# Performance work log

Hardware: AMD Instinct MI355X
Metric: run time of the kernel (lower is better)

The kernel has to match this reference:

```python
import jax, jax.numpy as jnp
import numpy as np

S = 14
STEP = 1.0 / S
LAMBDA_COORD = 7.0
LAMBDA_NOOBJ = 0.2
LAMBDA_CLS = 1.5
EPS = 1e-06


def _abs_coords(boxes):
    # boxes: [N, S, S, 2, 5] -> [N, S, S, 2, 4] (x1,y1,x2,y2)
    ys, xs = jnp.meshgrid(jnp.arange(S, dtype=boxes.dtype), jnp.arange(S, dtype=boxes.dtype), indexing='ij')
    xg = xs[None, :, :, None]
    yg = ys[None, :, :, None]
    cx = (boxes[..., 0] + xg) * STEP
    cy = (boxes[..., 1] + yg) * STEP
    w = boxes[..., 2]
    h = boxes[..., 3]
    return jnp.stack([cx - w / 2, cy - h / 2, cx + w / 2, cy + h / 2], axis=-1)


def _iou(b1, b2):
    x1 = jnp.maximum(b1[..., 0], b2[..., 0])
    y1 = jnp.maximum(b1[..., 1], b2[..., 1])
    x2 = jnp.minimum(b1[..., 2], b2[..., 2])
    y2 = jnp.minimum(b1[..., 3], b2[..., 3])
    inter = jnp.clip(x2 - x1, 0) * jnp.clip(y2 - y1, 0)
    a1 = (b1[..., 2] - b1[..., 0]) * (b1[..., 3] - b1[..., 1])
    a2 = (b2[..., 2] - b2[..., 0]) * (b2[..., 3] - b2[..., 1])
    return inter / (a1 + a2 - inter + EPS)


def _ciou_loss(b1, b2):
    iou = _iou(b1, b2)
    cx1 = (b1[..., 0] + b1[..., 2]) / 2
    cy1 = (b1[..., 1] + b1[..., 3]) / 2
    cx2 = (b2[..., 0] + b2[..., 2]) / 2
    cy2 = (b2[..., 1] + b2[..., 3]) / 2
    center_dist = (cx1 - cx2) ** 2 + (cy1 - cy2) ** 2
    xc1 = jnp.minimum(b1[..., 0], b2[..., 0])
    yc1 = jnp.minimum(b1[..., 1], b2[..., 1])
    xc2 = jnp.maximum(b1[..., 2], b2[..., 2])
    yc2 = jnp.maximum(b1[..., 3], b2[..., 3])
    outer_diag = (xc2 - xc1) ** 2 + (yc2 - yc1) ** 2 + EPS
    w1 = jnp.clip(b1[..., 2] - b1[..., 0], EPS)
    h1 = jnp.clip(b1[..., 3] - b1[..., 1], EPS)
    w2 = jnp.clip(b2[..., 2] - b2[..., 0], EPS)
    h2 = jnp.clip(b2[..., 3] - b2[..., 1], EPS)
    v = (4.0 / jnp.pi ** 2) * (jnp.arctan(w2 / h2) - jnp.arctan(w1 / h1)) ** 2
    alpha = v / (1 - iou + v + EPS)
    ciou = iou - center_dist / outer_diag - alpha * v
    scale = jnp.clip(2 - w2 * h2, 1.0)
    return (1 - ciou) * scale


def setup_inputs() -> dict:
    key = jax.random.key(0)
    k1, k2 = jax.random.split(key)
    N = 4096
    pred = jax.random.uniform(k1, (N, S, S, 30), dtype=jnp.float32)
    target = jax.random.uniform(k2, (N, S, S, 30), dtype=jnp.float32)
    return {"pred": pred, "target": target}


def reference(pred, target):
    N = pred.shape[0]
    tb = target[..., :10].reshape(N, S, S, 2, 5)
    pb = pred[..., :10].reshape(N, S, S, 2, 5)
    tcls = target[..., 10:]
    pcls = pred[..., 10:]

    obj = tb[..., 4] > 0                      # [N,S,S,2]
    pabs = _abs_coords(pb)                    # [N,S,S,2,4]
    tabs = _abs_coords(tb)

    # responsible-box assignment: IoU of both pred boxes vs target box 0
    ious = _iou(pabs, tabs[..., 0:1, :])      # [N,S,S,2]
    max_i = jnp.argmax(ious, axis=-1)         # first-max tie-break, same as torch
    resp = max_i[..., None] == jnp.arange(2)  # [N,S,S,2] bool
    obj = obj & resp
    noobj = ~obj

    pconf = pb[..., 4]
    tconf = tb[..., 4]
    se = (pconf - tconf) ** 2
    noobj_loss = jnp.sum(se * noobj)
    obj_loss = jnp.sum(se * obj)

    bbox_loss = jnp.sum(_ciou_loss(pabs, tabs) * obj)

    sig = jnp.any(obj, axis=-1)               # [N,S,S]
    # torch F.binary_cross_entropy clamps log terms at -100
    logp = jnp.clip(jnp.log(pcls), -100.0)
    log1mp = jnp.clip(jnp.log1p(-pcls), -100.0)
    bce = -(tcls * logp + (1 - tcls) * log1mp)
    class_loss = jnp.sum(bce * sig[..., None]) * LAMBDA_CLS

    loss = obj_loss + LAMBDA_NOOBJ * noobj_loss + LAMBDA_COORD * bbox_loss + class_loss
    return loss / N
```

## Files before the change

### kernel.cpp

```cpp
#include <hip/hip_runtime.h>
#include <math.h>

namespace {
constexpr int SG = 14;
constexpr int NCELLS = 4096 * SG * SG;
constexpr int CPB = 64;
constexpr int NBLK = NCELLS / CPB;
constexpr int NBINS = 1024;
constexpr int BYTES_PER_BLK = CPB * 30 * 4;
constexpr float STEPF = 1.0f / 14.0f;
constexpr float EPSF = 1e-6f;
constexpr float L_COORD = 7.0f;
constexpr float L_NOOBJ = 0.2f;
constexpr float L_CLS = 1.5f;
constexpr float INV_N = 1.0f / 4096.0f;
constexpr float FOUR_OVER_PI2 = 4.0f / (float)(M_PI * M_PI);
}

#define AS1 __attribute__((address_space(1)))
#define AS3 __attribute__((address_space(3)))

__device__ __forceinline__ void gl_lds16(const void* g, void* l) {
  __builtin_amdgcn_global_load_lds((const AS1 unsigned int*)g, (AS3 unsigned int*)l, 16, 0, 0);
}
__device__ __forceinline__ void gl_lds4(const void* g, void* l) {
  __builtin_amdgcn_global_load_lds((const AS1 unsigned int*)g, (AS3 unsigned int*)l, 4, 0, 0);
}

struct Box { float x1, y1, x2, y2; };

__device__ __forceinline__ float iou_fn(const Box& a, const Box& b) {
  float ix1 = fmaxf(a.x1, b.x1);
  float iy1 = fmaxf(a.y1, b.y1);
  float ix2 = fminf(a.x2, b.x2);
  float iy2 = fminf(a.y2, b.y2);
  float inter = fmaxf(ix2 - ix1, 0.0f) * fmaxf(iy2 - iy1, 0.0f);
  float a1 = (a.x2 - a.x1) * (a.y2 - a.y1);
  float a2 = (b.x2 - b.x1) * (b.y2 - b.y1);
  return __fdividef(inter, a1 + a2 - inter + EPSF);
}

__device__ __forceinline__ float bce_term(float pc, float tc) {
  const float lg   = fmaxf(__logf(pc), -100.0f);
  const float l1mp = fmaxf(__logf(1.0f - pc), -100.0f);
  return -(tc * lg + (1.0f - tc) * l1mp);
}

__global__ __launch_bounds__(64) void yolo_k1(const float* __restrict__ pred,
                                              const float* __restrict__ tgt,
                                              float* __restrict__ bins) {
  __shared__ __align__(16) float pb[CPB * 30];
  __shared__ __align__(16) float tb[CPB * 30];

  const int lane = threadIdx.x;
  const size_t base = (size_t)blockIdx.x * BYTES_PER_BLK;
  const char* gp = (const char*)pred + base;
  const char* gt = (const char*)tgt + base;
  char* lp = (char*)pb;
  char* lt = (char*)tb;

#pragma unroll
  for (int j = 0; j < 7; ++j) {
    gl_lds16(gp + j * 1024 + lane * 16, lp + j * 1024);
    gl_lds16(gt + j * 1024 + lane * 16, lt + j * 1024);
  }
#pragma unroll
  for (int j = 0; j < 2; ++j) {
    gl_lds4(gp + 7168 + j * 256 + lane * 4, lp + 7168 + j * 256);
    gl_lds4(gt + 7168 + j * 256 + lane * 4, lt + 7168 + j * 256);
  }
  asm volatile("s_waitcnt vmcnt(0)" ::: "memory");

  const float2* pl = reinterpret_cast<const float2*>(pb + lane * 30);
  const float2* tl = reinterpret_cast<const float2*>(tb + lane * 30);

  float p[10], t[10];
#pragma unroll
  for (int k = 0; k < 5; ++k) {
    const float2 v = pl[k]; p[2 * k] = v.x; p[2 * k + 1] = v.y;
    const float2 u = tl[k]; t[2 * k] = u.x; t[2 * k + 1] = u.y;
  }

  const int cell = blockIdx.x * CPB + lane;
  const int rem = cell % (SG * SG);
  const float gx = (float)(rem % SG);
  const float gy = (float)(rem / SG);

  Box pa0, pa1, ta0, ta1;
  {
    float cx = (p[0] + gx) * STEPF, cy = (p[1] + gy) * STEPF, w = p[2], h = p[3];
    pa0 = {cx - 0.5f * w, cy - 0.5f * h, cx + 0.5f * w, cy + 0.5f * h};
    cx = (p[5] + gx) * STEPF; cy = (p[6] + gy) * STEPF; w = p[7]; h = p[8];
    pa1 = {cx - 0.5f * w, cy - 0.5f * h, cx + 0.5f * w, cy + 0.5f * h};
    cx = (t[0] + gx) * STEPF; cy = (t[1] + gy) * STEPF; w = t[2]; h = t[3];
    ta0 = {cx - 0.5f * w, cy - 0.5f * h, cx + 0.5f * w, cy + 0.5f * h};
    cx = (t[5] + gx) * STEPF; cy = (t[6] + gy) * STEPF; w = t[7]; h = t[8];
    ta1 = {cx - 0.5f * w, cy - 0.5f * h, cx + 0.5f * w, cy + 0.5f * h};
  }

  const float iou0 = iou_fn(pa0, ta0);
  const float iou1 = iou_fn(pa1, ta0);
  const bool m1 = iou1 > iou0;
  const bool obj0 = (t[4] > 0.0f) && !m1;
  const bool obj1 = (t[9] > 0.0f) && m1;
  const bool sig = obj0 || obj1;

  const float d0 = p[4] - t[4], d1 = p[9] - t[9];
  const float se0 = d0 * d0, se1 = d1 * d1;
  const float obj_loss   = (obj0 ? se0 : 0.0f) + (obj1 ? se1 : 0.0f);
  const float noobj_loss = (obj0 ? 0.0f : se0) + (obj1 ? 0.0f : se1);

  Box b1, b2;
  b1.x1 = m1 ? pa1.x1 : pa0.x1; b1.y1 = m1 ? pa1.y1 : pa0.y1;
  b1.x2 = m1 ? pa1.x2 : pa0.x2; b1.y2 = m1 ? pa1.y2 : pa0.y2;
  b2.x1 = m1 ? ta1.x1 : ta0.x1; b2.y1 = m1 ? ta1.y1 : ta0.y1;
  b2.x2 = m1 ? ta1.x2 : ta0.x2; b2.y2 = m1 ? ta1.y2 : ta0.y2;

  float bbox;
  {
    const float iou = iou_fn(b1, b2);
    const float cx1 = 0.5f * (b1.x1 + b1.x2), cy1 = 0.5f * (b1.y1 + b1.y2);
    const float cx2 = 0.5f * (b2.x1 + b2.x2), cy2 = 0.5f * (b2.y1 + b2.y2);
    const float cd = (cx1 - cx2) * (cx1 - cx2) + (cy1 - cy2) * (cy1 - cy2);
    const float ox1 = fminf(b1.x1, b2.x1), oy1 = fminf(b1.y1, b2.y1);
    const float ox2 = fmaxf(b1.x2, b2.x2), oy2 = fmaxf(b1.y2, b2.y2);
    const float od = (ox2 - ox1) * (ox2 - ox1) + (oy2 - oy1) * (oy2 - oy1) + EPSF;
    const float w1 = fmaxf(b1.x2 - b1.x1, EPSF), h1 = fmaxf(b1.y2 - b1.y1, EPSF);
    const float w2 = fmaxf(b2.x2 - b2.x1, EPSF), h2 = fmaxf(b2.y2 - b2.y1, EPSF);
    const float dat = atanf(__fdividef(w2, h2)) - atanf(__fdividef(w1, h1));
    const float v = FOUR_OVER_PI2 * dat * dat;
    const float alpha = __fdividef(v, 1.0f - iou + v + EPSF);
    const float ciou = iou - __fdividef(cd, od) - alpha * v;
    const float scale = fmaxf(2.0f - w2 * h2, 1.0f);
    bbox = sig ? (1.0f - ciou) * scale : 0.0f;
  }

  float cls = 0.0f;
#pragma unroll
  for (int k = 0; k < 10; ++k) {
    const float2 v = pl[5 + k];
    const float2 u = tl[5 + k];
    cls += bce_term(v.x, u.x) + bce_term(v.y, u.y);
  }

  float acc = obj_loss + L_NOOBJ * noobj_loss + L_COORD * bbox
            + (sig ? L_CLS * cls : 0.0f);

#pragma unroll
  for (int off = 32; off > 0; off >>= 1) acc += __shfl_down(acc, off);
  if (lane == 0) atomicAdd(&bins[blockIdx.x & (NBINS - 1)], acc);
}

__global__ __launch_bounds__(256) void yolo_k2(const float* __restrict__ bins,
                                               float* __restrict__ out) {
  const int tid = threadIdx.x;
  float s = bins[tid] + bins[tid + 256] + bins[tid + 512] + bins[tid + 768];
#pragma unroll
  for (int off = 32; off > 0; off >>= 1) s += __shfl_down(s, off);
  __shared__ float sd[4];
  if ((tid & 63) == 0) sd[tid >> 6] = s;
  __syncthreads();
  if (tid == 0) out[0] = (sd[0] + sd[1] + sd[2] + sd[3]) * INV_N;
}

extern "C" void kernel_launch(void* const* d_in, const int* in_sizes, int n_in,
                              void* d_out, int out_size, void* d_ws, size_t ws_size,
                              hipStream_t stream) {
  const float* pred = (const float*)d_in[0];
  const float* tgt  = (const float*)d_in[1];
  float* out  = (float*)d_out;
  float* bins = (float*)d_ws;

  hipMemsetAsync(bins, 0, NBINS * sizeof(float), stream);
  yolo_k1<<<NBLK, CPB, 0, stream>>>(pred, tgt, bins);
  yolo_k2<<<1, 256, 0, stream>>>(bins, out);
}
```

Baseline: 207.2 us.

## Use persistent double-buffered blocks with async LDS prefetch and polynomial atan

Replaces the one-tile-per-block launch with a fixed grid of 1280 persistent single-wave blocks. Each block loops over tiles and prefetches the next tile into a second LDS buffer with global_load_lds, waiting with a partial vmcnt so compute overlaps the loads. It also swaps atanf for a min/max range-reduced minimax polynomial. The cost is fewer resident waves per CU to hide latency, more LDS per block, and a small accuracy change in the atan term.

```diff
diff --git a/kernel.cpp b/kernel.cpp
--- a/kernel.cpp
+++ b/kernel.cpp
@@ -4,10 +4,10 @@
 namespace {
 constexpr int SG = 14;
 constexpr int NCELLS = 4096 * SG * SG;
-constexpr int CPB = 64;
-constexpr int NBLK = NCELLS / CPB;
-constexpr int NBINS = 1024;
-constexpr int BYTES_PER_BLK = CPB * 30 * 4;
+constexpr int CPT = 64;
+constexpr int NTILES = NCELLS / CPT;
+constexpr int GRID = 1280;
+constexpr int TILE_BYTES = CPT * 30 * 4;
 constexpr float STEPF = 1.0f / 14.0f;
 constexpr float EPSF = 1e-6f;
 constexpr float L_COORD = 7.0f;
@@ -15,6 +15,7 @@
 constexpr float L_CLS = 1.5f;
 constexpr float INV_N = 1.0f / 4096.0f;
 constexpr float FOUR_OVER_PI2 = 4.0f / (float)(M_PI * M_PI);
+constexpr float PI_OVER_2 = 1.57079632679489662f;
 }
 
 #define AS1 __attribute__((address_space(1)))
@@ -25,6 +26,20 @@
 }
 __device__ __forceinline__ void gl_lds4(const void* g, void* l) {
   __builtin_amdgcn_global_load_lds((const AS1 unsigned int*)g, (AS3 unsigned int*)l, 4, 0, 0);
+}
+
+__device__ __forceinline__ void stage_tile(const char* gp, const char* gt,
+                                           char* lp, char* lt, int lane) {
+#pragma unroll
+  for (int j = 0; j < 7; ++j) {
+    gl_lds16(gp + j * 1024 + lane * 16, lp + j * 1024);
+    gl_lds16(gt + j * 1024 + lane * 16, lt + j * 1024);
+  }
+#pragma unroll
+  for (int j = 0; j < 2; ++j) {
+    gl_lds4(gp + 7168 + j * 256 + lane * 4, lp + 7168 + j * 256);
+    gl_lds4(gt + 7168 + j * 256 + lane * 4, lt + 7168 + j * 256);
+  }
 }
 
 struct Box { float x1, y1, x2, y2; };
@@ -40,39 +55,30 @@
   return __fdividef(inter, a1 + a2 - inter + EPSF);
 }
 
+__device__ __forceinline__ float atan_ratio(float w, float h) {
+  const float mn = fminf(w, h), mx = fmaxf(w, h);
+  const float a = __fdividef(mn, mx);
+  const float s = a * a;
+  float r = -0.01172120f;
+  r = r * s + 0.05265332f;
+  r = r * s + -0.11643287f;
+  r = r * s + 0.19354346f;
+  r = r * s + -0.33262347f;
+  r = r * s + 0.99997726f;
+  r = r * a;
+  return (w > h) ? (PI_OVER_2 - r) : r;
+}
+
 __device__ __forceinline__ float bce_term(float pc, float tc) {
   const float lg   = fmaxf(__logf(pc), -100.0f);
   const float l1mp = fmaxf(__logf(1.0f - pc), -100.0f);
   return -(tc * lg + (1.0f - tc) * l1mp);
 }
 
-__global__ __launch_bounds__(64) void yolo_k1(const float* __restrict__ pred,
-                                              const float* __restrict__ tgt,
-                                              float* __restrict__ bins) {
-  __shared__ __align__(16) float pb[CPB * 30];
-  __shared__ __align__(16) float tb[CPB * 30];
-
-  const int lane = threadIdx.x;
-  const size_t base = (size_t)blockIdx.x * BYTES_PER_BLK;
-  const char* gp = (const char*)pred + base;
-  const char* gt = (const char*)tgt + base;
-  char* lp = (char*)pb;
-  char* lt = (char*)tb;
-
-#pragma unroll
-  for (int j = 0; j < 7; ++j) {
-    gl_lds16(gp + j * 1024 + lane * 16, lp + j * 1024);
-    gl_lds16(gt + j * 1024 + lane * 16, lt + j * 1024);
-  }
-#pragma unroll
-  for (int j = 0; j < 2; ++j) {
-    gl_lds4(gp + 7168 + j * 256 + lane * 4, lp + 7168 + j * 256);
-    gl_lds4(gt + 7168 + j * 256 + lane * 4, lt + 7168 + j * 256);
-  }
-  asm volatile("s_waitcnt vmcnt(0)" ::: "memory");
-
-  const float2* pl = reinterpret_cast<const float2*>(pb + lane * 30);
-  const float2* tl = reinterpret_cast<const float2*>(tb + lane * 30);
+__device__ __forceinline__ float cell_loss(const float* pbase, const float* tbase,
+                                           int lane, int cell) {
+  const float2* pl = reinterpret_cast<const float2*>(pbase + lane * 30);
+  const float2* tl = reinterpret_cast<const float2*>(tbase + lane * 30);
 
   float p[10], t[10];
 #pragma unroll
@@ -81,7 +87,6 @@
     const float2 u = tl[k]; t[2 * k] = u.x; t[2 * k + 1] = u.y;
   }
 
-  const int cell = blockIdx.x * CPB + lane;
   const int rem = cell % (SG * SG);
   const float gx = (float)(rem % SG);
   const float gy = (float)(rem / SG);
@@ -127,7 +132,7 @@
     const float od = (ox2 - ox1) * (ox2 - ox1) + (oy2 - oy1) * (oy2 - oy1) + EPSF;
     const float w1 = fmaxf(b1.x2 - b1.x1, EPSF), h1 = fmaxf(b1.y2 - b1.y1, EPSF);
     const float w2 = fmaxf(b2.x2 - b2.x1, EPSF), h2 = fmaxf(b2.y2 - b2.y1, EPSF);
-    const float dat = atanf(__fdividef(w2, h2)) - atanf(__fdividef(w1, h1));
+    const float dat = atan_ratio(w2, h2) - atan_ratio(w1, h1);
     const float v = FOUR_OVER_PI2 * dat * dat;
     const float alpha = __fdividef(v, 1.0f - iou + v + EPSF);
     const float ciou = iou - __fdividef(cd, od) - alpha * v;
@@ -143,18 +148,50 @@
     cls += bce_term(v.x, u.x) + bce_term(v.y, u.y);
   }
 
-  float acc = obj_loss + L_NOOBJ * noobj_loss + L_COORD * bbox
-            + (sig ? L_CLS * cls : 0.0f);
+  return obj_loss + L_NOOBJ * noobj_loss + L_COORD * bbox
+       + (sig ? L_CLS * cls : 0.0f);
+}
+
+__global__ __launch_bounds__(64) void yolo_k1(const float* __restrict__ pred,
+                                              const float* __restrict__ tgt,
+                                              float* __restrict__ bins) {
+  __shared__ __align__(16) float buf[2][2][CPT * 30];
+
+  const int lane = threadIdx.x;
+  const int bid = blockIdx.x;
+  const char* pc = (const char*)pred;
+  const char* tc = (const char*)tgt;
+
+  float acc = 0.0f;
+  int cur = 0;
+
+  stage_tile(pc + (size_t)bid * TILE_BYTES, tc + (size_t)bid * TILE_BYTES,
+             (char*)&buf[0][0][0], (char*)&buf[0][1][0], lane);
+
+  for (int t = bid; t < NTILES; t += GRID) {
+    const int tn = t + GRID;
+    if (tn < NTILES) {
+      stage_tile(pc + (size_t)tn * TILE_BYTES, tc + (size_t)tn * TILE_BYTES,
+                 (char*)&buf[cur ^ 1][0][0], (char*)&buf[cur ^ 1][1][0], lane);
+      asm volatile("s_waitcnt vmcnt(18)" ::: "memory");
+    } else {
+      asm volatile("s_waitcnt vmcnt(0)" ::: "memory");
+    }
+    acc += cell_loss(&buf[cur][0][0], &buf[cur][1][0], lane, t * CPT + lane);
+    cur ^= 1;
+  }
 
 #pragma unroll
   for (int off = 32; off > 0; off >>= 1) acc += __shfl_down(acc, off);
-  if (lane == 0) atomicAdd(&bins[blockIdx.x & (NBINS - 1)], acc);
+  if (lane == 0) atomicAdd(&bins[bid], acc);
 }
 
 __global__ __launch_bounds__(256) void yolo_k2(const float* __restrict__ bins,
                                                float* __restrict__ out) {
   const int tid = threadIdx.x;
-  float s = bins[tid] + bins[tid + 256] + bins[tid + 512] + bins[tid + 768];
+  float s = 0.0f;
+#pragma unroll
+  for (int i = 0; i < GRID / 256; ++i) s += bins[tid + 256 * i];
 #pragma unroll
   for (int off = 32; off > 0; off >>= 1) s += __shfl_down(s, off);
   __shared__ float sd[4];
@@ -171,7 +208,7 @@
   float* out  = (float*)d_out;
   float* bins = (float*)d_ws;
 
-  hipMemsetAsync(bins, 0, NBINS * sizeof(float), stream);
-  yolo_k1<<<NBLK, CPB, 0, stream>>>(pred, tgt, bins);
+  hipMemsetAsync(bins, 0, GRID * sizeof(float), stream);
+  yolo_k1<<<GRID, CPT, 0, stream>>>(pred, tgt, bins);
   yolo_k2<<<1, 256, 0, stream>>>(bins, out);
 }
```

Result: no change. 210.3 us (+1.5%).
